# Kernel optimization log

Hardware: AMD Instinct MI355X
Metric: run time of the kernel (lower is better)

The kernel has to match this reference:

```python
import jax, jax.numpy as jnp
import numpy as np

B, S, NQ, H, HD = 2, 4096, 576, 32, 128
HID = H * HD  # 4096


def setup_inputs() -> dict:
    key = jax.random.key(0)
    ks = jax.random.split(key, 7)
    sc = 0.02
    return {
        "hidden_states": jax.random.normal(ks[0], (B, S, HID), jnp.float32),
        "by_pass_hidden_states": jax.random.normal(ks[1], (B, NQ, HID), jnp.float32),
        "attention_mask": jnp.zeros((B, 1, S, NQ), jnp.float32),
        "Wq": jax.random.normal(ks[2], (HID, HID), jnp.float32) * sc,
        "Wk": jax.random.normal(ks[3], (HID, HID), jnp.float32) * sc,
        "Wv": jax.random.normal(ks[4], (HID, HID), jnp.float32) * sc,
        "Wo": jax.random.normal(ks[5], (HID, HID), jnp.float32) * sc,
    }


def reference(hidden_states, by_pass_hidden_states, attention_mask, Wq, Wk, Wv, Wo):
    b, s, _ = hidden_states.shape
    nq = by_pass_hidden_states.shape[1]
    # projections (nn.Linear applies x @ W.T); reshape to (b, heads, len, head_dim)
    q = (hidden_states @ Wq.T).reshape(b, s, H, HD).transpose(0, 2, 1, 3)
    k = (by_pass_hidden_states @ Wk.T).reshape(b, nq, H, HD).transpose(0, 2, 1, 3)
    v = (by_pass_hidden_states @ Wv.T).reshape(b, nq, H, HD).transpose(0, 2, 1, 3)
    # eager QK^T -> mask -> fp32 softmax -> V
    scores = jnp.einsum("bhsd,bhqd->bhsq", q, k) / jnp.sqrt(jnp.float32(HD))
    scores = scores + attention_mask  # (b,1,s,nq) broadcast over heads
    attn = jax.nn.softmax(scores.astype(jnp.float32), axis=-1).astype(q.dtype)
    out = jnp.einsum("bhsq,bhqd->bhsd", attn, v)
    out = out.transpose(0, 2, 1, 3).reshape(b, s, HID)
    return out @ Wo.T
```

## Files before the change

### kernel.cpp

```cpp
#include <hip/hip_runtime.h>
#include <stdint.h>

#define Bn   2
#define Sn   4096
#define NQn  576
#define Hn   32
#define HDn  128
#define HIDn 4096

typedef unsigned short bfu;
typedef short short8 __attribute__((ext_vector_type(8)));
typedef float f32x4 __attribute__((ext_vector_type(4)));

__device__ __forceinline__ bfu f2b(float f) {
  uint32_t x = __builtin_bit_cast(uint32_t, f);
  return (bfu)((x + 0x7fffu + ((x >> 16) & 1u)) >> 16);
}

__device__ __forceinline__ void gload16(const void* g, void* l) {
  __builtin_amdgcn_global_load_lds(
      (const __attribute__((address_space(1))) uint32_t*)g,
      (__attribute__((address_space(3))) uint32_t*)l, 16, 0, 0);
}

__global__ void cast_f32_bf16(const float* __restrict__ in, bfu* __restrict__ out,
                              int n8) {
  int i = blockIdx.x * 256 + threadIdx.x;
  if (i >= n8) return;
  const float4* in4 = (const float4*)in;
  float4 a = in4[2 * i], c = in4[2 * i + 1];
  short8 v;
  v[0] = (short)f2b(a.x); v[1] = (short)f2b(a.y);
  v[2] = (short)f2b(a.z); v[3] = (short)f2b(a.w);
  v[4] = (short)f2b(c.x); v[5] = (short)f2b(c.y);
  v[6] = (short)f2b(c.z); v[7] = (short)f2b(c.w);
  ((short8*)out)[i] = v;
}

template <int WRITE_BF16>
__global__ __launch_bounds__(512, 2)
void gemm_bt256(const bfu* __restrict__ A, const bfu* __restrict__ Bm,
                void* __restrict__ Cout, int M, int N, int K) {
  __shared__ __align__(16) bfu Asm[2][256 * 64];
  __shared__ __align__(16) bfu Bsm[2][256 * 64];
  const int tid = threadIdx.x;
  const int wave = tid >> 6, lane = tid & 63;
  const int lr = lane & 15, kq = lane >> 4;
  const int wm = wave >> 2, wn = wave & 3;
  const long m0 = (long)blockIdx.y * 256, n0 = (long)blockIdx.x * 256;
  const int NT = K >> 6;

  const int c0j = tid >> 3, c0c = tid & 7;
  const int c1j = (512 + tid) >> 3, c1c = tid & 7;
  const bfu* aSrc0 = A + (m0 + c0j) * (long)K + ((c0c ^ (c0j & 7)) * 8);
  const bfu* aSrc1 = A + (m0 + c1j) * (long)K + ((c1c ^ (c1j & 7)) * 8);
  const bfu* bSrc0 = Bm + (n0 + c0j) * (long)K + ((c0c ^ (c0j & 7)) * 8);
  const bfu* bSrc1 = Bm + (n0 + c1j) * (long)K + ((c1c ^ (c1j & 7)) * 8);

  auto stageA = [&](int t, int buf, int half) {
    long koff = (long)t * 64 + (long)half * 128 * K;
    gload16(aSrc0 + koff, &Asm[buf][half * 8192 + (wave * 64) * 8]);
    gload16(aSrc1 + koff, &Asm[buf][half * 8192 + (512 + wave * 64) * 8]);
  };
  auto stageB = [&](int t, int buf, int half) {
    long koff = (long)t * 64 + (long)half * 128 * K;
    gload16(bSrc0 + koff, &Bsm[buf][half * 8192 + (wave * 64) * 8]);
    gload16(bSrc1 + koff, &Bsm[buf][half * 8192 + (512 + wave * 64) * 8]);
  };
  auto ldsA = [&](int buf, int mf, int ks) -> short8 {
    int row = (mf >> 2) * 128 + wm * 64 + (mf & 3) * 16 + lr;
    int off = (row * 128 + ks * 64 + kq * 16) ^ ((row & 7) << 4);
    return *(const short8*)((const char*)Asm[buf] + off);
  };
  auto ldsB = [&](int buf, int nf, int ks) -> short8 {
    int row = (nf >> 1) * 128 + wn * 32 + (nf & 1) * 16 + lr;
    int off = (row * 128 + ks * 64 + kq * 16) ^ ((row & 7) << 4);
    return *(const short8*)((const char*)Bsm[buf] + off);
  };

  f32x4 acc[8][4] = {};
  short8 a0[4][2], a1[4][2], b0[2][2], b1[2][2];

#define MFMA16(MB, NB, AA, BB)                                                  \
  _Pragma("unroll") for (int mf = 0; mf < 4; ++mf)                              \
      _Pragma("unroll") for (int ks = 0; ks < 2; ++ks)                          \
      _Pragma("unroll") for (int nf = 0; nf < 2; ++nf)                          \
      acc[MB + mf][NB + nf] = __builtin_amdgcn_mfma_f32_16x16x32_bf16(          \
          AA[mf][ks], BB[nf][ks], acc[MB + mf][NB + nf], 0, 0, 0);

  stageA(0, 0, 0); stageB(0, 0, 0); stageB(0, 0, 1); stageA(0, 0, 1);
  stageA(1, 1, 0); stageB(1, 1, 0); stageB(1, 1, 1); stageA(1, 1, 1);
  asm volatile("s_waitcnt vmcnt(6)" ::: "memory");
  __builtin_amdgcn_s_barrier();

  for (int tp = 0; tp < NT; tp += 2) {
    const bool more = (tp + 2 < NT);
#pragma unroll
    for (int hh = 0; hh < 2; ++hh) {
      const int bb = hh;
      const int ts = tp + hh + 2;
#pragma unroll
      for (int mf = 0; mf < 4; ++mf) {
        a0[mf][0] = ldsA(bb, mf, 0);
        a0[mf][1] = ldsA(bb, mf, 1);
      }
#pragma unroll
      for (int nf = 0; nf < 2; ++nf) {
        b0[nf][0] = ldsB(bb, nf, 0);
        b0[nf][1] = ldsB(bb, nf, 1);
      }
      asm volatile("s_waitcnt lgkmcnt(8)" ::: "memory");
      __builtin_amdgcn_s_barrier();
      asm volatile("s_waitcnt lgkmcnt(0)" ::: "memory");
      __builtin_amdgcn_s_setprio(1);
      MFMA16(0, 0, a0, b0)
      __builtin_amdgcn_s_setprio(0);
      __builtin_amdgcn_s_barrier();
#pragma unroll
      for (int nf = 0; nf < 2; ++nf) {
        b1[nf][0] = ldsB(bb, 2 + nf, 0);
        b1[nf][1] = ldsB(bb, 2 + nf, 1);
      }
      if (more) { stageA(ts, bb, 0); stageB(ts, bb, 0); }
      __builtin_amdgcn_s_barrier();
      asm volatile("s_waitcnt lgkmcnt(0)" ::: "memory");
      __builtin_amdgcn_s_setprio(1);
      MFMA16(0, 2, a0, b1)
      __builtin_amdgcn_s_setprio(0);
      __builtin_amdgcn_s_barrier();
#pragma unroll
      for (int mf = 0; mf < 4; ++mf) {
        a1[mf][0] = ldsA(bb, 4 + mf, 0);
        a1[mf][1] = ldsA(bb, 4 + mf, 1);
      }
      if (more) stageB(ts, bb, 1);
      __builtin_amdgcn_s_barrier();
      asm volatile("s_waitcnt lgkmcnt(0)" ::: "memory");
      __builtin_amdgcn_s_setprio(1);
      MFMA16(4, 2, a1, b1)
      __builtin_amdgcn_s_setprio(0);
      __builtin_amdgcn_s_barrier();
      if (more) stageA(ts, bb, 1);
      __builtin_amdgcn_s_barrier();
      __builtin_amdgcn_s_setprio(1);
      MFMA16(4, 0, a1, b0)
      __builtin_amdgcn_s_setprio(0);
      if (more) {
        asm volatile("s_waitcnt vmcnt(6)" ::: "memory");
      } else if (hh == 0) {
        asm volatile("s_waitcnt vmcnt(0)" ::: "memory");
      }
      __builtin_amdgcn_s_barrier();
    }
  }
#undef MFMA16

#pragma unroll
  for (int mf = 0; mf < 8; ++mf)
#pragma unroll
    for (int nf = 0; nf < 4; ++nf)
#pragma unroll
      for (int r = 0; r < 4; ++r) {
        long row = m0 + (mf >> 2) * 128 + wm * 64 + (mf & 3) * 16 + kq * 4 + r;
        long col = n0 + (nf >> 1) * 128 + wn * 32 + (nf & 1) * 16 + lr;
        float v = acc[mf][nf][r];
        if (WRITE_BF16)
          ((bfu*)Cout)[row * N + col] = f2b(v);
        else
          ((float*)Cout)[row * N + col] = v;
      }
}

template <int WRITE_BF16>
__global__ __launch_bounds__(256, 2)
void gemm_bt(const bfu* __restrict__ A, const bfu* __restrict__ Bm,
             void* __restrict__ Cout, int M, int N, int K) {
  __shared__ __align__(16) bfu As[128 * 32];
  __shared__ __align__(16) bfu Bs[128 * 32];
  const int tid = threadIdx.x;
  const int wave = tid >> 6, lane = tid & 63;
  const int lr = lane & 15, kq = lane >> 4;
  const int wm = wave >> 1, wn = wave & 1;
  const long m0 = (long)blockIdx.y * 128, n0 = (long)blockIdx.x * 128;

  f32x4 acc[4][4] = {};

  for (int kk = 0; kk < K; kk += 32) {
#pragma unroll
    for (int i = 0; i < 2; ++i) {
      int tt = i * 256 + tid;
      long row = tt >> 2;
      int col = (tt & 3) * 8;
      gload16(A + (m0 + row) * K + kk + col, &As[(i * 256 + wave * 64) * 8]);
      gload16(Bm + (n0 + row) * K + kk + col, &Bs[(i * 256 + wave * 64) * 8]);
    }
    __syncthreads();
    short8 a[4], b[4];
#pragma unroll
    for (int mt = 0; mt < 4; ++mt)
      a[mt] = *(const short8*)&As[(wm * 64 + mt * 16 + lr) * 32 + kq * 8];
#pragma unroll
    for (int nt = 0; nt < 4; ++nt)
      b[nt] = *(const short8*)&Bs[(wn * 64 + nt * 16 + lr) * 32 + kq * 8];
#pragma unroll
    for (int mt = 0; mt < 4; ++mt)
#pragma unroll
      for (int nt = 0; nt < 4; ++nt)
        acc[mt][nt] = __builtin_amdgcn_mfma_f32_16x16x32_bf16(
            a[mt], b[nt], acc[mt][nt], 0, 0, 0);
    __syncthreads();
  }
#pragma unroll
  for (int mt = 0; mt < 4; ++mt)
#pragma unroll
    for (int nt = 0; nt < 4; ++nt)
#pragma unroll
      for (int r = 0; r < 4; ++r) {
        long row = m0 + wm * 64 + mt * 16 + kq * 4 + r;
        long col = n0 + wn * 64 + nt * 16 + lr;
        float v = acc[mt][nt][r];
        if (WRITE_BF16)
          ((bfu*)Cout)[row * N + col] = f2b(v);
        else
          ((float*)Cout)[row * N + col] = v;
      }
}

__global__ void transpose_v(const bfu* __restrict__ KVb, bfu* __restrict__ Vt) {
  __shared__ bfu t[32][33];
  const int bh = blockIdx.z;
  const int tq = blockIdx.x;
  const int td = blockIdx.y;
  const int b = bh >> 5, h = bh & 31;
  const int tx = threadIdx.x & 31, ty = threadIdx.x >> 5;
  const bfu* src =
      KVb + ((long)(b * NQn + tq * 32)) * 8192 + 4096 + h * HDn + td * 32;
#pragma unroll
  for (int i = 0; i < 32; i += 8) t[ty + i][tx] = src[(long)(ty + i) * 8192 + tx];
  __syncthreads();
  bfu* dst = Vt + ((long)bh * HDn + td * 32) * NQn + tq * 32;
#pragma unroll
  for (int i = 0; i < 32; i += 8) dst[(long)(ty + i) * NQn + tx] = t[tx][ty + i];
}

__global__ __launch_bounds__(256, 4)
void attn_kernel(const bfu* __restrict__ Qb, const bfu* __restrict__ KVb,
                 const bfu* __restrict__ Vt, const float* __restrict__ mask,
                 bfu* __restrict__ AO) {
  __shared__ __align__(16) bfu Ks[2][4096];
  __shared__ __align__(16) bfu Vs[2][4096];
  const int bid = blockIdx.x;
  const int h = bid & (Hn - 1);
  const int b = (bid >> 5) & (Bn - 1);
  const int qt0 = bid >> 6;
  const long q0 = (long)qt0 * 64;
  const int tid = threadIdx.x;
  const int wave = tid >> 6, lane = tid & 63;
  const int lr = lane & 15, kq = lane >> 4;
  const float scale = 0.08838834764831845f;

  const long qrow = (long)b * Sn + q0 + wave * 16 + lr;
  const bfu* Kblk = KVb + (long)b * NQn * 8192 + h * HDn;
  const bfu* Vblk = Vt + ((long)(b * Hn + h)) * HDn * NQn;
  const float* mrow = mask + ((long)b * Sn + q0 + wave * 16 + lr) * NQn;

  auto stageK = [&](int kt, int buf) {
#pragma unroll
    for (int i = 0; i < 2; ++i) {
      int c = i * 256 + tid;
      int j = c >> 4, c16 = c & 15;
      gload16(Kblk + (long)(kt * 32 + j) * 8192 + ((c16 ^ (j & 7)) * 8),
              &Ks[buf][(i * 256 + wave * 64) * 8]);
    }
  };
  auto stageV = [&](int kt, int buf) {
#pragma unroll
    for (int i = 0; i < 2; ++i) {
      int c = i * 256 + tid;
      int j = c >> 2, c4 = c & 3;
      gload16(Vblk + (long)j * NQn + kt * 32 + c4 * 8,
              &Vs[buf][(i * 256 + wave * 64) * 8]);
    }
  };

  stageK(0, 0);
  stageV(0, 0);

  const bfu* Qbase = Qb + qrow * HIDn + h * HDn;
  short8 qf[4];
#pragma unroll
  for (int ks = 0; ks < 4; ++ks)
    qf[ks] = *(const short8*)&Qbase[ks * 32 + kq * 8];

  f32x4 o[8] = {};
  float rsum = 0.f;

  for (int kt = 0; kt < 18; ++kt) {
    __syncthreads();
    const int buf = kt & 1;
    if (kt < 17) {
      stageK(kt + 1, buf ^ 1);
      stageV(kt + 1, buf ^ 1);
    }
    const char* kb = (const char*)Ks[buf];
    f32x4 s0 = {}, s1 = {};
#pragma unroll
    for (int ks = 0; ks < 4; ++ks) {
      short8 kf0 = *(const short8*)(kb + ((lr * 256 + ks * 64 + kq * 16) ^
                                          ((lr & 7) << 4)));
      short8 kf1 = *(const short8*)(kb + (((16 + lr) * 256 + ks * 64 + kq * 16) ^
                                          ((lr & 7) << 4)));
      s0 = __builtin_amdgcn_mfma_f32_16x16x32_bf16(kf0, qf[ks], s0, 0, 0, 0);
      s1 = __builtin_amdgcn_mfma_f32_16x16x32_bf16(kf1, qf[ks], s1, 0, 0, 0);
    }
    float4 m0 = *(const float4*)&mrow[kt * 32 + kq * 4];
    float4 m1 = *(const float4*)&mrow[kt * 32 + 16 + kq * 4];
    float p00 = __expf(s0[0] * scale + m0.x), p01 = __expf(s0[1] * scale + m0.y);
    float p02 = __expf(s0[2] * scale + m0.z), p03 = __expf(s0[3] * scale + m0.w);
    float p10 = __expf(s1[0] * scale + m1.x), p11 = __expf(s1[1] * scale + m1.y);
    float p12 = __expf(s1[2] * scale + m1.z), p13 = __expf(s1[3] * scale + m1.w);
    rsum += ((p00 + p01) + (p02 + p03)) + ((p10 + p11) + (p12 + p13));
    int pk0_0 = (int)((uint32_t)f2b(p00) | ((uint32_t)f2b(p01) << 16));
    int pk0_1 = (int)((uint32_t)f2b(p02) | ((uint32_t)f2b(p03) << 16));
    int pk1_0 = (int)((uint32_t)f2b(p10) | ((uint32_t)f2b(p11) << 16));
    int pk1_1 = (int)((uint32_t)f2b(p12) | ((uint32_t)f2b(p13) << 16));
    const int sLo = lr + (((kq & 1) << 1) << 4);
    const int sHi = sLo + 16;
    int b0, b1, b2, b3;
    {
      int v0 = __shfl(pk0_0, sLo, 64), v1 = __shfl(pk1_0, sLo, 64);
      b0 = (kq < 2) ? v0 : v1;
      v0 = __shfl(pk0_1, sLo, 64); v1 = __shfl(pk1_1, sLo, 64);
      b1 = (kq < 2) ? v0 : v1;
      v0 = __shfl(pk0_0, sHi, 64); v1 = __shfl(pk1_0, sHi, 64);
      b2 = (kq < 2) ? v0 : v1;
      v0 = __shfl(pk0_1, sHi, 64); v1 = __shfl(pk1_1, sHi, 64);
      b3 = (kq < 2) ? v0 : v1;
    }
    int4 pfi = {b0, b1, b2, b3};
    short8 pfrag = __builtin_bit_cast(short8, pfi);
    const char* vb = (const char*)Vs[buf];
#pragma unroll
    for (int dt = 0; dt < 8; ++dt) {
      short8 vf = *(const short8*)(vb + ((dt * 16 + lr) * 64 + kq * 16));
      o[dt] = __builtin_amdgcn_mfma_f32_16x16x32_bf16(vf, pfrag, o[dt], 0, 0, 0);
    }
  }

  rsum += __shfl_xor(rsum, 16, 64);
  rsum += __shfl_xor(rsum, 32, 64);
  const float inv = 1.0f / rsum;

  bfu* Obase = AO + qrow * HIDn + h * HDn;
#pragma unroll
  for (int dt = 0; dt < 8; ++dt) {
    uint64_t pk = (uint64_t)f2b(o[dt][0] * inv) |
                  ((uint64_t)f2b(o[dt][1] * inv) << 16) |
                  ((uint64_t)f2b(o[dt][2] * inv) << 32) |
                  ((uint64_t)f2b(o[dt][3] * inv) << 48);
    *(uint64_t*)&Obase[dt * 16 + kq * 4] = pk;
  }
}

extern "C" void kernel_launch(void* const* d_in, const int* in_sizes, int n_in,
                              void* d_out, int out_size, void* d_ws, size_t ws_size,
                              hipStream_t stream) {
  const float* hs = (const float*)d_in[0];
  const float* bp = (const float*)d_in[1];
  const float* mask = (const float*)d_in[2];
  const float* Wq = (const float*)d_in[3];
  const float* Wk = (const float*)d_in[4];
  const float* Wv = (const float*)d_in[5];
  const float* Wo = (const float*)d_in[6];
  float* out = (float*)d_out;

  const long M1 = (long)Bn * Sn;
  const long M2 = (long)Bn * NQn;
  char* ws = (char*)d_ws;
  bfu* hb = (bfu*)(ws + 0);
  bfu* bb = (bfu*)(ws + 67108864);
  bfu* w1 = (bfu*)(ws + 76546048);
  bfu* wkv = (bfu*)(ws + 110100480);
  bfu* Qb = (bfu*)(ws + 177209344);
  bfu* KVb = (bfu*)(ws + 244318208);
  bfu* Vt = (bfu*)(ws + 263192576);

  auto cast = [&](const float* src, bfu* dst, long n) {
    int n8 = (int)(n / 8);
    cast_f32_bf16<<<dim3((n8 + 255) / 256), dim3(256), 0, stream>>>(src, dst, n8);
  };
  cast(hs, hb, M1 * HIDn);
  cast(bp, bb, M2 * HIDn);
  cast(Wq, w1, (long)HIDn * HIDn);
  cast(Wk, wkv, (long)HIDn * HIDn);
  cast(Wv, wkv + (long)HIDn * HIDn, (long)HIDn * HIDn);

  gemm_bt256<1><<<dim3(HIDn / 256, M1 / 256), dim3(512), 0, stream>>>(
      hb, w1, Qb, (int)M1, HIDn, HIDn);
  gemm_bt<1><<<dim3(8192 / 128, M2 / 128), dim3(256), 0, stream>>>(
      bb, wkv, KVb, (int)M2, 8192, HIDn);

  cast(Wo, w1, (long)HIDn * HIDn);
  transpose_v<<<dim3(NQn / 32, HDn / 32, Bn * Hn), dim3(256), 0, stream>>>(
      KVb, Vt);

  attn_kernel<<<dim3((Sn / 64) * Bn * Hn), dim3(256), 0, stream>>>(
      Qb, KVb, Vt, mask, hb );

  gemm_bt256<0><<<dim3(HIDn / 256, M1 / 256), dim3(512), 0, stream>>>(
      hb, w1, out, (int)M1, HIDn, HIDn);
}
```

Measured before the change: 896.4 us.

## Merge input casts into one launch and trim GEMM LDS barriers

Replaces five separate f32-to-bf16 cast launches with one kernel that walks all five buffers by flat index, cutting launch overhead. In the 256-tile GEMM main loop, LDS fragment reads for the next MFMA group are issued earlier. Several barriers and explicit lgkmcnt waits are dropped, leaving more LDS latency overlapped with MFMA work. Removing the barriers and waits relies on compiler-inserted waits for correctness and risks races between staging writes and fragment reads on the double buffer.

```diff
diff --git a/kernel.cpp b/kernel.cpp
--- a/kernel.cpp
+++ b/kernel.cpp
@@ -23,18 +23,37 @@
       (__attribute__((address_space(3))) uint32_t*)l, 16, 0, 0);
 }
 
-__global__ void cast_f32_bf16(const float* __restrict__ in, bfu* __restrict__ out,
-                              int n8) {
-  int i = blockIdx.x * 256 + threadIdx.x;
-  if (i >= n8) return;
-  const float4* in4 = (const float4*)in;
+__device__ __forceinline__ void cast8(const float* s, bfu* d, long i) {
+  const float4* in4 = (const float4*)s;
   float4 a = in4[2 * i], c = in4[2 * i + 1];
   short8 v;
   v[0] = (short)f2b(a.x); v[1] = (short)f2b(a.y);
   v[2] = (short)f2b(a.z); v[3] = (short)f2b(a.w);
   v[4] = (short)f2b(c.x); v[5] = (short)f2b(c.y);
   v[6] = (short)f2b(c.z); v[7] = (short)f2b(c.w);
-  ((short8*)out)[i] = v;
+  ((short8*)d)[i] = v;
+}
+
+__global__ void cast_f32_bf16(const float* __restrict__ in, bfu* __restrict__ out,
+                              int n8) {
+  long i = (long)blockIdx.x * 256 + threadIdx.x;
+  if (i >= n8) return;
+  cast8(in, out, i);
+}
+
+__global__ void cast5(const float* s0, bfu* d0, int n0, const float* s1, bfu* d1,
+                      int n1, const float* s2, bfu* d2, int n2, const float* s3,
+                      bfu* d3, int n3, const float* s4, bfu* d4, int n4) {
+  long gid = (long)blockIdx.x * 256 + threadIdx.x;
+  if (gid < n0) { cast8(s0, d0, gid); return; }
+  gid -= n0;
+  if (gid < n1) { cast8(s1, d1, gid); return; }
+  gid -= n1;
+  if (gid < n2) { cast8(s2, d2, gid); return; }
+  gid -= n2;
+  if (gid < n3) { cast8(s3, d3, gid); return; }
+  gid -= n3;
+  if (gid < n4) cast8(s4, d4, gid);
 }
 
 template <int WRITE_BF16>
@@ -109,39 +128,31 @@
         b0[nf][0] = ldsB(bb, nf, 0);
         b0[nf][1] = ldsB(bb, nf, 1);
       }
-      asm volatile("s_waitcnt lgkmcnt(8)" ::: "memory");
-      __builtin_amdgcn_s_barrier();
-      asm volatile("s_waitcnt lgkmcnt(0)" ::: "memory");
+#pragma unroll
+      for (int nf = 0; nf < 2; ++nf) {
+        b1[nf][0] = ldsB(bb, 2 + nf, 0);
+        b1[nf][1] = ldsB(bb, 2 + nf, 1);
+      }
       __builtin_amdgcn_s_setprio(1);
       MFMA16(0, 0, a0, b0)
       __builtin_amdgcn_s_setprio(0);
       __builtin_amdgcn_s_barrier();
 #pragma unroll
-      for (int nf = 0; nf < 2; ++nf) {
-        b1[nf][0] = ldsB(bb, 2 + nf, 0);
-        b1[nf][1] = ldsB(bb, 2 + nf, 1);
+      for (int mf = 0; mf < 4; ++mf) {
+        a1[mf][0] = ldsA(bb, 4 + mf, 0);
+        a1[mf][1] = ldsA(bb, 4 + mf, 1);
       }
       if (more) { stageA(ts, bb, 0); stageB(ts, bb, 0); }
-      __builtin_amdgcn_s_barrier();
-      asm volatile("s_waitcnt lgkmcnt(0)" ::: "memory");
       __builtin_amdgcn_s_setprio(1);
       MFMA16(0, 2, a0, b1)
       __builtin_amdgcn_s_setprio(0);
       __builtin_amdgcn_s_barrier();
-#pragma unroll
-      for (int mf = 0; mf < 4; ++mf) {
-        a1[mf][0] = ldsA(bb, 4 + mf, 0);
-        a1[mf][1] = ldsA(bb, 4 + mf, 1);
-      }
       if (more) stageB(ts, bb, 1);
-      __builtin_amdgcn_s_barrier();
-      asm volatile("s_waitcnt lgkmcnt(0)" ::: "memory");
       __builtin_amdgcn_s_setprio(1);
       MFMA16(4, 2, a1, b1)
       __builtin_amdgcn_s_setprio(0);
       __builtin_amdgcn_s_barrier();
       if (more) stageA(ts, bb, 1);
-      __builtin_amdgcn_s_barrier();
       __builtin_amdgcn_s_setprio(1);
       MFMA16(4, 0, a1, b0)
       __builtin_amdgcn_s_setprio(0);
@@ -385,22 +396,21 @@
   bfu* KVb = (bfu*)(ws + 244318208);
   bfu* Vt = (bfu*)(ws + 263192576);
 
-  auto cast = [&](const float* src, bfu* dst, long n) {
-    int n8 = (int)(n / 8);
-    cast_f32_bf16<<<dim3((n8 + 255) / 256), dim3(256), 0, stream>>>(src, dst, n8);
-  };
-  cast(hs, hb, M1 * HIDn);
-  cast(bp, bb, M2 * HIDn);
-  cast(Wq, w1, (long)HIDn * HIDn);
-  cast(Wk, wkv, (long)HIDn * HIDn);
-  cast(Wv, wkv + (long)HIDn * HIDn, (long)HIDn * HIDn);
+  const int n8_hs = (int)(M1 * HIDn / 8);
+  const int n8_bp = (int)(M2 * HIDn / 8);
+  const int n8_w = (int)((long)HIDn * HIDn / 8);
+  const long tot8 = (long)n8_hs + n8_bp + 3L * n8_w;
+  cast5<<<dim3((int)(tot8 / 256)), dim3(256), 0, stream>>>(
+      hs, hb, n8_hs, bp, bb, n8_bp, Wq, w1, n8_w, Wk, wkv, n8_w, Wv,
+      wkv + (long)HIDn * HIDn, n8_w);
 
   gemm_bt256<1><<<dim3(HIDn / 256, M1 / 256), dim3(512), 0, stream>>>(
       hb, w1, Qb, (int)M1, HIDn, HIDn);
   gemm_bt<1><<<dim3(8192 / 128, M2 / 128), dim3(256), 0, stream>>>(
       bb, wkv, KVb, (int)M2, 8192, HIDn);
 
-  cast(Wo, w1, (long)HIDn * HIDn);
+  cast_f32_bf16<<<dim3(n8_w / 256), dim3(256), 0, stream>>>(
+      Wo, w1, n8_w);
   transpose_v<<<dim3(NQn / 32, HDn / 32, Bn * Hn), dim3(256), 0, stream>>>(
       KVb, Vt);
 
```

Result: slower. 1.190 ms (+32.8%).
